# Performance work log

Hardware: AMD Instinct MI355X
Metric: run time of the kernel (lower is better)

## Reference

```python
import jax, jax.numpy as jnp
import numpy as np

NUM_HEADS = 12


def setup_inputs() -> dict:
    key = jax.random.key(0)
    k1, k2, k3, k4 = jax.random.split(key, 4)
    B, N, C = 32, 577, 768
    x = jax.random.normal(k1, (B, N, C), dtype=jnp.float32)
    qkv_w = jax.random.normal(k2, (3 * C, C), dtype=jnp.float32) * 0.02
    proj_w = jax.random.normal(k3, (C, C), dtype=jnp.float32) * 0.02
    proj_b = jax.random.normal(k4, (C,), dtype=jnp.float32) * 0.02
    return {"x": x, "qkv_w": qkv_w, "proj_w": proj_w, "proj_b": proj_b,
            "reduction_num": 115}


def reference(x, qkv_w, proj_w, proj_b, reduction_num):
    B, N, C = x.shape
    H = NUM_HEADS
    hd = C // H
    scale = hd ** -0.5

    # qkv projection (no bias), split into q, k, v of shape (B, H, N, hd)
    qkv = (x @ qkv_w.T).reshape(B, N, 3, H, hd)
    qkv = jnp.transpose(qkv, (2, 0, 3, 1, 4))  # (3, B, H, N, hd)
    q, k, v = qkv[0], qkv[1], qkv[2]

    attn = jax.nn.softmax(jnp.einsum('bhnd,bhmd->bhnm', q * scale, k), axis=-1)  # (B,H,N,N)

    # diagonal entries at positions 1..N-1 (skip CLS), averaged over heads
    attn_diag = jnp.diagonal(attn, axis1=-2, axis2=-1)[:, :, 1:].mean(axis=1)  # (B, N-1)

    token_rank = jnp.argsort(-attn_diag, axis=1)  # descending
    num_kept = N - reduction_num
    kept = token_rank[:, : N - 1 - reduction_num] + 1  # token indices (non-CLS)
    index_cls = jnp.zeros((B, 1), dtype=kept.dtype)
    index_kept = jnp.sort(jnp.concatenate([index_cls, kept], axis=1), axis=1)  # (B, num_kept)

    # gather kept query rows of the attention matrix: (B, H, num_kept, N)
    weight = jnp.take_along_axis(attn, index_kept[:, None, :, None], axis=2)

    out = jnp.einsum('bhkn,bhnd->bhkd', weight, v)  # (B, H, num_kept, hd)
    out = jnp.transpose(out, (0, 2, 1, 3)).reshape(B, num_kept, C)
    out = out @ proj_w.T + proj_b

    original_x = jnp.take_along_axis(x, index_kept[:, :, None], axis=1)  # (B, num_kept, C)
    return out + original_x
```

## Files before the change

### kernel.cpp

```cpp
#include <hip/hip_runtime.h>
#include <math.h>

#define BB_   32
#define NN_   577
#define CC_   768
#define HH_   12
#define HD_   64
#define NPAD  640
#define BH_   (BB_*HH_)
#define MQ    (BB_*NN_)
#define KEPT  462
#define KEPTP 464
#define MP    (BB_*KEPT)
#define TOPK  461

#define MT_   145
#define NT_   18

using short8 = __attribute__((ext_vector_type(8))) short;
using f32x4  = __attribute__((ext_vector_type(4))) float;
using u16x4  = __attribute__((ext_vector_type(4))) unsigned short;
using u32x2  = __attribute__((ext_vector_type(2))) unsigned int;

using gp1_t = const __attribute__((address_space(1))) void*;
using sp3_t = __attribute__((address_space(3))) void*;

__device__ __forceinline__ unsigned short f2bf(float f) {
  unsigned int u = __float_as_uint(f);
  u += 0x7fffu + ((u >> 16) & 1u);
  return (unsigned short)(u >> 16);
}
__device__ __forceinline__ float bf2f(unsigned short h) {
  return __uint_as_float(((unsigned int)h) << 16);
}
__device__ __forceinline__ f32x4 mfma16(short8 a, short8 b, f32x4 c) {
  return __builtin_amdgcn_mfma_f32_16x16x32_bf16(a, b, c, 0, 0, 0);
}
__device__ __forceinline__ void gl_lds16(const void* g, void* l) {
  __builtin_amdgcn_global_load_lds((gp1_t)g, (sp3_t)l, 16, 0, 0);
}

#define SC_ 0.18033688011112042f

__device__ __forceinline__ void split4(const float* __restrict__ in, int i,
                                       unsigned short* __restrict__ hi,
                                       unsigned short* __restrict__ lo) {
  f32x4 f = *(const f32x4*)(in + (size_t)i * 4);
  u16x4 hv, lv;
#pragma unroll
  for (int j = 0; j < 4; ++j) {
    unsigned short h = f2bf(f[j]);
    hv[j] = h;
    lv[j] = f2bf(f[j] - bf2f(h));
  }
  *(u16x4*)(hi + (size_t)i * 4) = hv;
  if (lo) *(u16x4*)(lo + (size_t)i * 4) = lv;
}

#define NX4_ (MQ * 768 / 4)
#define NW4_ (2304 * 768 / 4)
#define NP4_ (768 * 768 / 4)

__global__ __launch_bounds__(256) void k_split_all(
    const float* __restrict__ x, const float* __restrict__ qw,
    const float* __restrict__ pw,
    unsigned short* __restrict__ xh, unsigned short* __restrict__ xl,
    unsigned short* __restrict__ wh, unsigned short* __restrict__ wl,
    unsigned short* __restrict__ pwh) {
  int i = blockIdx.x * 256 + threadIdx.x;
  if (i < NX4_) {
    split4(x, i, xh, xl);
  } else if (i < NX4_ + NW4_) {
    split4(qw, i - NX4_, wh, wl);
  } else if (i < NX4_ + NW4_ + NP4_) {
    split4(pw, i - NX4_ - NW4_, pwh, (unsigned short*)nullptr);
  }
}

__global__ __launch_bounds__(256, 2) void k_qkv(
    const unsigned short* __restrict__ xh, const unsigned short* __restrict__ xl,
    const unsigned short* __restrict__ wh, const unsigned short* __restrict__ wl,
    unsigned short* __restrict__ qh, unsigned short* __restrict__ ql,
    unsigned short* __restrict__ kh, unsigned short* __restrict__ kl,
    unsigned short* __restrict__ vt) {
  __shared__ char smem[65536];
  unsigned short* lAh = (unsigned short*)smem;
  unsigned short* lAl = (unsigned short*)(smem + 16384);
  unsigned short* lBh = (unsigned short*)(smem + 32768);
  unsigned short* lBl = (unsigned short*)(smem + 49152);

  const int tid = threadIdx.x;
  const int wave = tid >> 6, lane = tid & 63, lr = lane & 15, lg = lane >> 4;
  const int wm = wave >> 1, wn = wave & 1;

  const int nwg = MT_ * NT_;
  const int qq = nwg >> 3, rr = nwg & 7;
  int orig = blockIdx.x;
  int xcd = orig & 7, pos = orig >> 3;
  int wgid = (xcd < rr ? xcd * (qq + 1) : rr * (qq + 1) + (xcd - rr) * qq) + pos;
  const int mt = wgid / NT_, nt = wgid - mt * NT_;
  const int m0 = mt * 128, n0 = nt * 128;
  const int which = n0 / 768;
  const bool three = (which < 2);

  f32x4 zf = {0.f, 0.f, 0.f, 0.f};
  f32x4 acc[4][4];
#pragma unroll
  for (int a = 0; a < 4; ++a)
#pragma unroll
    for (int bq = 0; bq < 4; ++bq) acc[a][bq] = zf;

  for (int ks = 0; ks < 12; ++ks) {
    const int k0 = ks * 64;
#pragma unroll
    for (int it = 0; it < 4; ++it) {
      int c = it * 256 + tid;
      int row = c >> 3, slot = c & 7;
      int grow = m0 + row; if (grow > MQ - 1) grow = MQ - 1;
      int gk = k0 + ((slot ^ (row & 7)) << 3);
      gl_lds16(xh + (size_t)grow * 768 + gk,
               (char*)lAh + (it * 256 + wave * 64) * 16);
      if (three)
        gl_lds16(xl + (size_t)grow * 768 + gk,
                 (char*)lAl + (it * 256 + wave * 64) * 16);
    }
#pragma unroll
    for (int it = 0; it < 4; ++it) {
      int c = it * 256 + tid;
      int row = c >> 3, slot = c & 7;
      int gn = n0 + row;
      int gk = k0 + ((slot ^ (row & 7)) << 3);
      gl_lds16(wh + (size_t)gn * 768 + gk,
               (char*)lBh + (it * 256 + wave * 64) * 16);
      if (three)
        gl_lds16(wl + (size_t)gn * 768 + gk,
                 (char*)lBl + (it * 256 + wave * 64) * 16);
    }
    __syncthreads();

#pragma unroll
    for (int kk = 0; kk < 2; ++kk) {
      short8 fa[4], fal[4], fb[4], fbl[4];
#pragma unroll
      for (int ms = 0; ms < 4; ++ms) {
        int row = wm * 64 + ms * 16 + lr;
        int off = (kk * 64 + lg * 16) ^ ((row & 7) << 4);
        fa[ms] = *(const short8*)((const char*)lAh + row * 128 + off);
        if (three) fal[ms] = *(const short8*)((const char*)lAl + row * 128 + off);
      }
#pragma unroll
      for (int ns = 0; ns < 4; ++ns) {
        int row = wn * 64 + ns * 16 + lr;
        int off = (kk * 64 + lg * 16) ^ ((row & 7) << 4);
        fb[ns] = *(const short8*)((const char*)lBh + row * 128 + off);
        if (three) fbl[ns] = *(const short8*)((const char*)lBl + row * 128 + off);
      }
#pragma unroll
      for (int ms = 0; ms < 4; ++ms)
#pragma unroll
        for (int ns = 0; ns < 4; ++ns) {
          acc[ms][ns] = mfma16(fa[ms], fb[ns], acc[ms][ns]);
          if (three) {
            acc[ms][ns] = mfma16(fa[ms], fbl[ns], acc[ms][ns]);
            acc[ms][ns] = mfma16(fal[ms], fb[ns], acc[ms][ns]);
          }
        }
    }
    __syncthreads();
  }

  if (which < 2) {
    float* lC = (float*)smem;
    for (int p = 0; p < 2; ++p) {
      if (p) __syncthreads();
      if (wn == p) {
#pragma unroll
        for (int ms = 0; ms < 4; ++ms)
#pragma unroll
          for (int ns = 0; ns < 4; ++ns) {
            int r = wm * 64 + ms * 16 + 4 * lg;
            int cc = ns * 16 + lr;
#pragma unroll
            for (int reg = 0; reg < 4; ++reg)
              lC[(r + reg) * 66 + cc] = acc[ms][ns][reg];
          }
      }
      __syncthreads();
      const int h = ((n0 % 768) >> 6) + p;
      int r = tid >> 1, c0 = (tid & 1) * 32;
      int m = m0 + r;
      if (m < MQ) {
        int b = m / 577, n = m % 577;
        size_t base = ((size_t)(b * 12 + h) * NPAD + n) * 64 + c0;
        unsigned short* dh = (which == 0 ? qh : kh) + base;
        unsigned short* dl = (which == 0 ? ql : kl) + base;
#pragma unroll
        for (int cc = 0; cc < 32; cc += 4) {
          u16x4 hv, lv;
#pragma unroll
          for (int j = 0; j < 4; ++j) {
            float f = lC[r * 66 + c0 + cc + j];
            unsigned short hh = f2bf(f);
            hv[j] = hh;
            lv[j] = f2bf(f - bf2f(hh));
          }
          *(u16x4*)(dh + cc) = hv;
          *(u16x4*)(dl + cc) = lv;
        }
      }
    }
  } else {
    const int h0 = (n0 % 768) >> 6;
#pragma unroll
    for (int ms = 0; ms < 4; ++ms)
#pragma unroll
      for (int ns = 0; ns < 4; ++ns) {
        int m = m0 + wm * 64 + ms * 16 + 4 * lg;
        int c = wn * 64 + ns * 16 + lr;
        int h = h0 + (c >> 6), d = c & 63;
        int b = m / 577, n = m - b * 577;
        if (m + 3 < MQ && n + 3 < 577) {
          u16x4 pv;
#pragma unroll
          for (int reg = 0; reg < 4; ++reg) pv[reg] = f2bf(acc[ms][ns][reg]);
          *(u16x4*)(vt + ((size_t)(b * 12 + h) * 64 + d) * NPAD + n) = pv;
        } else {
#pragma unroll
          for (int reg = 0; reg < 4; ++reg) {
            int mm = m + reg;
            if (mm < MQ) {
              int bb = mm / 577, nn = mm - bb * 577;
              vt[((size_t)(bb * 12 + h) * 64 + d) * NPAD + nn] = f2bf(acc[ms][ns][reg]);
            }
          }
        }
      }
  }
}

__global__ __launch_bounds__(256) void k_attn1(
    const unsigned short* __restrict__ qh, const unsigned short* __restrict__ ql,
    const unsigned short* __restrict__ kh, const unsigned short* __restrict__ kl,
    const unsigned short* __restrict__ vt, float* __restrict__ S0,
    float* __restrict__ Dg, unsigned short* __restrict__ Ob) {
  __shared__ char smem[34816];
  char* lK = smem;
  char* lV = smem + 16384;
  char* lP = smem + 24576;

  int wgid = (blockIdx.x & 7) * 480 + (blockIdx.x >> 3);
  const int bh = wgid / 10;
  const int i0 = (wgid - bh * 10) * 64;
  const int tid = threadIdx.x, w = tid >> 6, lane = tid & 63;
  const int lr = lane & 15, lg = lane >> 4;
  const size_t qb = (size_t)bh * NPAD * 64;

  const int krow = tid >> 3, kslot = tid & 7;
  const int vrow = tid >> 2, vslot = tid & 3;
  const size_t ksrc = (size_t)krow * 64 + ((kslot ^ (krow & 7)) << 3);
  const size_t vsrc = ((size_t)bh * 64 + vrow) * NPAD + ((vslot ^ (vrow & 3)) << 3);

  short8 qf[2], qfl[2];
  {
    const size_t qrow = qb + (size_t)(i0 + w * 16 + lr) * 64;
#pragma unroll
    for (int kk = 0; kk < 2; ++kk) {
      qf[kk]  = *(const short8*)(qh + qrow + kk * 32 + lg * 8);
      qfl[kk] = *(const short8*)(ql + qrow + kk * 32 + lg * 8);
    }
  }
  f32x4 zf = {0.f, 0.f, 0.f, 0.f};
  f32x4 oacc[4];
#pragma unroll
  for (int ds = 0; ds < 4; ++ds) oacc[ds] = zf;
  float s0 = 0.0f;

  gl_lds16(kh + qb + ksrc, lK + tid * 16);
  gl_lds16(kl + qb + ksrc, lK + 4096 + tid * 16);
  gl_lds16(vt + vsrc, lV + tid * 16);
  __syncthreads();

  int buf = 0, pb = 0;
  char* lPw = lP + w * 2560;
  for (int jp = 0; jp < 19; ++jp) {
    if (jp < 18) {
      int jn = (jp + 1) * 32;
      gl_lds16(kh + qb + (size_t)jn * 64 + ksrc, lK + (buf ^ 1) * 8192 + tid * 16);
      gl_lds16(kl + qb + (size_t)jn * 64 + ksrc, lK + (buf ^ 1) * 8192 + 4096 + tid * 16);
      gl_lds16(vt + vsrc + jn, lV + (buf ^ 1) * 4096 + tid * 16);
    }
#pragma unroll
    for (int t = 0; t < 2; ++t) {
      const int jloc = t * 16 + lr;
      short8 kfh[2], kfl2[2];
#pragma unroll
      for (int kk = 0; kk < 2; ++kk) {
        int off = (kk * 64 + lg * 16) ^ ((jloc & 7) << 4);
        kfh[kk]  = *(const short8*)(lK + buf * 8192 + jloc * 128 + off);
        kfl2[kk] = *(const short8*)(lK + buf * 8192 + 4096 + jloc * 128 + off);
      }
      f32x4 c = zf;
#pragma unroll
      for (int kk = 0; kk < 2; ++kk) {
        c = mfma16(kfh[kk], qfl[kk], c);
        c = mfma16(kfl2[kk], qf[kk], c);
        c = mfma16(kfh[kk], qf[kk], c);
      }
      int jbase = jp * 32 + t * 16 + 4 * lg;
      float p0 = (jbase + 0 < 577) ? exp2f(c[0] * SC_) : 0.0f;
      float p1 = (jbase + 1 < 577) ? exp2f(c[1] * SC_) : 0.0f;
      float p2 = (jbase + 2 < 577) ? exp2f(c[2] * SC_) : 0.0f;
      float p3 = (jbase + 3 < 577) ? exp2f(c[3] * SC_) : 0.0f;
      s0 += (p0 + p1) + (p2 + p3);
      u32x2 wv;
      wv[0] = (unsigned)f2bf(p0) | ((unsigned)f2bf(p1) << 16);
      wv[1] = (unsigned)f2bf(p2) | ((unsigned)f2bf(p3) << 16);
      *(u32x2*)(lPw + pb * 1280 + lr * 80 + t * 32 + lg * 8) = wv;
    }
    asm volatile("" ::: "memory");
    short8 pa = *(const short8*)(lPw + pb * 1280 + lr * 80 + lg * 16);
#pragma unroll
    for (int ds = 0; ds < 4; ++ds) {
      int r = ds * 16 + lr;
      int off = (lg * 16) ^ ((r & 3) << 4);
      short8 vf = *(const short8*)(lV + buf * 4096 + r * 64 + off);
      oacc[ds] = mfma16(pa, vf, oacc[ds]);
    }
    asm volatile("" ::: "memory");
    pb ^= 1;
    __syncthreads();
    buf ^= 1;
  }

  s0 += __shfl_xor(s0, 16);
  s0 += __shfl_xor(s0, 32);
  const int iw = i0 + w * 16;
  if (lg == 0) S0[(size_t)bh * NPAD + iw + lr] = s0;
  float rs[4];
#pragma unroll
  for (int reg = 0; reg < 4; ++reg) rs[reg] = 1.0f / __shfl(s0, 4 * lg + reg);
#pragma unroll
  for (int ds = 0; ds < 4; ++ds)
#pragma unroll
    for (int reg = 0; reg < 4; ++reg)
      Ob[((size_t)bh * NPAD + iw + 4 * lg + reg) * 64 + ds * 16 + lr] =
          f2bf(oacc[ds][reg] * rs[reg]);

  {
    const int row = i0 + (tid >> 2);
    const int c = tid & 3;
    const size_t base = qb + (size_t)row * 64 + c * 16;
    short8 a0 = *(const short8*)(qh + base), a1 = *(const short8*)(qh + base + 8);
    short8 b0 = *(const short8*)(ql + base), b1 = *(const short8*)(ql + base + 8);
    short8 c0 = *(const short8*)(kh + base), c1 = *(const short8*)(kh + base + 8);
    short8 d0 = *(const short8*)(kl + base), d1 = *(const short8*)(kl + base + 8);
    float acc = 0.0f;
#pragma unroll
    for (int j = 0; j < 8; ++j) {
      float qv = bf2f((unsigned short)a0[j]) + bf2f((unsigned short)b0[j]);
      float kv = bf2f((unsigned short)c0[j]) + bf2f((unsigned short)d0[j]);
      acc += qv * kv;
      float qv1 = bf2f((unsigned short)a1[j]) + bf2f((unsigned short)b1[j]);
      float kv1 = bf2f((unsigned short)c1[j]) + bf2f((unsigned short)d1[j]);
      acc += qv1 * kv1;
    }
    acc += __shfl_xor(acc, 1, 4);
    acc += __shfl_xor(acc, 2, 4);
    if (c == 0) Dg[(size_t)bh * NPAD + row] = acc * SC_;
  }
}

__global__ __launch_bounds__(576) void k_select(const float* __restrict__ Dg,
                                                const float* __restrict__ S0,
                                                int* __restrict__ idxk) {
  __shared__ float kbuf[576];
  __shared__ int kflag[576];
  int b = blockIdx.x, t = threadIdx.x;
  if (t < 576) {
    float a = 0.0f;
#pragma unroll
    for (int h = 0; h < 12; ++h) {
      size_t o = (size_t)(b * 12 + h) * NPAD + t + 1;
      a += exp2f(Dg[o]) / S0[o];
    }
    kbuf[t] = a;
  }
  __syncthreads();
  if (t < 576) {
    float kt = kbuf[t];
    int cnt = 0;
    for (int j = 0; j < 576; ++j) {
      float kj = kbuf[j];
      cnt += (kj > kt || (kj == kt && j < t)) ? 1 : 0;
    }
    kflag[t] = (cnt < TOPK) ? 1 : 0;
  }
  __syncthreads();
  if (t < 576 && kflag[t]) {
    int pos = 1;
    for (int j = 0; j < t; ++j) pos += kflag[j];
    idxk[b * KEPTP + pos] = t + 1;
  }
  if (t == 0) {
    idxk[b * KEPTP + 0] = 0;
    idxk[b * KEPTP + 462] = 0;
    idxk[b * KEPTP + 463] = 0;
  }
}

__global__ __launch_bounds__(256) void k_proj(
    const unsigned short* __restrict__ Ob, const unsigned short* __restrict__ pwh,
    const float* __restrict__ pb, const float* __restrict__ x,
    const int* __restrict__ idxk, float* __restrict__ out) {
  __shared__ char smem[33792];
  unsigned short* lA = (unsigned short*)smem;
  unsigned short* lB = (unsigned short*)(smem + 16384);
  const int tid = threadIdx.x;
  const int wave = tid >> 6, lane = tid & 63, lr = lane & 15, lg = lane >> 4;
  const int wm = wave >> 1, wn = wave & 1;
  int wgid = (blockIdx.x & 7) * 87 + (blockIdx.x >> 3);
  const int mt = wgid / 6, nt = wgid - mt * 6;
  const int m0 = mt * 128, n0 = nt * 128;

  int tokr[4], bbr[4], offr8[4];
#pragma unroll
  for (int it = 0; it < 4; ++it) {
    int c = it * 256 + tid;
    int row = c >> 3, slot = c & 7;
    int m = m0 + row; if (m > MP - 1) m = MP - 1;
    int bb = m / 462, tt = m - bb * 462;
    tokr[it] = idxk[bb * KEPTP + tt];
    bbr[it] = bb;
    offr8[it] = (slot ^ (row & 7)) << 3;
  }

  f32x4 zf = {0.f, 0.f, 0.f, 0.f};
  f32x4 acc[4][4];
#pragma unroll
  for (int a = 0; a < 4; ++a)
#pragma unroll
    for (int bq = 0; bq < 4; ++bq) acc[a][bq] = zf;

  for (int ks = 0; ks < 12; ++ks) {
    int k0 = ks * 64;
#pragma unroll
    for (int it = 0; it < 4; ++it) {
      gl_lds16(Ob + ((size_t)(bbr[it] * 12 + ks) * NPAD + tokr[it]) * 64 + offr8[it],
               (char*)lA + (it * 256 + wave * 64) * 16);
    }
#pragma unroll
    for (int it = 0; it < 4; ++it) {
      int c = it * 256 + tid;
      int row = c >> 3, slot = c & 7;
      int gk = k0 + ((slot ^ (row & 7)) << 3);
      gl_lds16(pwh + (size_t)(n0 + row) * 768 + gk,
               (char*)lB + (it * 256 + wave * 64) * 16);
    }
    __syncthreads();
#pragma unroll
    for (int kk = 0; kk < 2; ++kk) {
      short8 fa[4], fb[4];
#pragma unroll
      for (int ms = 0; ms < 4; ++ms) {
        int row = wm * 64 + ms * 16 + lr;
        int off = (kk * 64 + lg * 16) ^ ((row & 7) << 4);
        fa[ms] = *(const short8*)((const char*)lA + row * 128 + off);
      }
#pragma unroll
      for (int ns = 0; ns < 4; ++ns) {
        int row = wn * 64 + ns * 16 + lr;
        int off = (kk * 64 + lg * 16) ^ ((row & 7) << 4);
        fb[ns] = *(const short8*)((const char*)lB + row * 128 + off);
      }
#pragma unroll
      for (int ms = 0; ms < 4; ++ms)
#pragma unroll
        for (int ns = 0; ns < 4; ++ns)
          acc[ms][ns] = mfma16(fa[ms], fb[ns], acc[ms][ns]);
    }
    __syncthreads();
  }

  float* lC = (float*)smem;
  for (int p = 0; p < 2; ++p) {
    if (p) __syncthreads();
    if (wn == p) {
#pragma unroll
      for (int ms = 0; ms < 4; ++ms)
#pragma unroll
        for (int ns = 0; ns < 4; ++ns) {
          int r = wm * 64 + ms * 16 + 4 * lg;
          int cc = ns * 16 + lr;
#pragma unroll
          for (int reg = 0; reg < 4; ++reg)
            lC[(r + reg) * 66 + cc] = acc[ms][ns][reg];
        }
    }
    __syncthreads();
    int r = tid >> 1, c0 = (tid & 1) * 32;
    int m = m0 + r;
    if (m < MP) {
      int bb = m / 462, tt = m % 462;
      int tok = idxk[bb * KEPTP + tt];
      int col = n0 + p * 64 + c0;
      const float* xs = x + ((size_t)(bb * 577) + tok) * 768 + col;
      float* dst = out + (size_t)m * 768 + col;
#pragma unroll
      for (int cc = 0; cc < 32; cc += 4) {
        f32x4 xv = *(const f32x4*)(xs + cc);
        f32x4 bv = *(const f32x4*)(pb + col + cc);
        f32x4 o;
#pragma unroll
        for (int j = 0; j < 4; ++j)
          o[j] = lC[r * 66 + c0 + cc + j] + bv[j] + xv[j];
        *(f32x4*)(dst + cc) = o;
      }
    }
  }
}

extern "C" void kernel_launch(void* const* d_in, const int* in_sizes, int n_in,
                              void* d_out, int out_size, void* d_ws, size_t ws_size,
                              hipStream_t stream) {
  const float* x  = (const float*)d_in[0];
  const float* qw = (const float*)d_in[1];
  const float* pw = (const float*)d_in[2];
  const float* pb = (const float*)d_in[3];
  (void)in_sizes; (void)n_in; (void)out_size; (void)ws_size;

  char* ws = (char*)d_ws;
  size_t off = 0;
  auto alloc = [&](size_t bytes) {
    void* p = ws + off;
    off += (bytes + 255) & ~(size_t)255;
    return p;
  };
  unsigned short* xh  = (unsigned short*)alloc((size_t)MQ * 768 * 2);
  unsigned short* xl  = (unsigned short*)alloc((size_t)MQ * 768 * 2);
  unsigned short* wh  = (unsigned short*)alloc((size_t)2304 * 768 * 2);
  unsigned short* wl  = (unsigned short*)alloc((size_t)2304 * 768 * 2);
  unsigned short* pwh = (unsigned short*)alloc((size_t)768 * 768 * 2);
  unsigned short* qhp = (unsigned short*)alloc((size_t)BH_ * NPAD * 64 * 2);
  unsigned short* qlp = (unsigned short*)alloc((size_t)BH_ * NPAD * 64 * 2);
  unsigned short* khp = (unsigned short*)alloc((size_t)BH_ * NPAD * 64 * 2);
  unsigned short* klp = (unsigned short*)alloc((size_t)BH_ * NPAD * 64 * 2);
  unsigned short* vtp = (unsigned short*)alloc((size_t)BH_ * NPAD * 64 * 2);
  unsigned short* Obf = (unsigned short*)alloc((size_t)BH_ * NPAD * 64 * 2);
  float* S0  = (float*)alloc((size_t)BH_ * NPAD * 4);
  float* Dg  = (float*)alloc((size_t)BH_ * NPAD * 4);
  int*   idxk = (int*)alloc((size_t)BB_ * KEPTP * 4);

  k_split_all<<<dim3((NX4_ + NW4_ + NP4_ + 255) / 256), 256, 0, stream>>>(
      x, qw, pw, xh, xl, wh, wl, pwh);
  k_qkv<<<dim3(MT_ * NT_), 256, 0, stream>>>(xh, xl, wh, wl, qhp, qlp, khp, klp, vtp);
  k_attn1<<<dim3(3840), 256, 0, stream>>>(qhp, qlp, khp, klp, vtp, S0, Dg, Obf);
  k_select<<<dim3(32), 576, 0, stream>>>(Dg, S0, idxk);
  k_proj<<<dim3(696), 256, 0, stream>>>(Obf, pwh, pb, x, idxk, (float*)d_out);
}
```

Baseline: 377.6 us.

## Double query rows per attention workgroup to reuse K/V tiles; two elements per split thread

After: 377.1 us, median of 3. About the same (-0.1%).

```diff
diff --git a/kernel.cpp b/kernel.cpp
--- a/kernel.cpp
+++ b/kernel.cpp
@@ -67,13 +67,17 @@
     unsigned short* __restrict__ xh, unsigned short* __restrict__ xl,
     unsigned short* __restrict__ wh, unsigned short* __restrict__ wl,
     unsigned short* __restrict__ pwh) {
-  int i = blockIdx.x * 256 + threadIdx.x;
-  if (i < NX4_) {
-    split4(x, i, xh, xl);
-  } else if (i < NX4_ + NW4_) {
-    split4(qw, i - NX4_, wh, wl);
-  } else if (i < NX4_ + NW4_ + NP4_) {
-    split4(pw, i - NX4_ - NW4_, pwh, (unsigned short*)nullptr);
+  int i2 = blockIdx.x * 256 + threadIdx.x;
+#pragma unroll
+  for (int s = 0; s < 2; ++s) {
+    int i = 2 * i2 + s;
+    if (i < NX4_) {
+      split4(x, i, xh, xl);
+    } else if (i < NX4_ + NW4_) {
+      split4(qw, i - NX4_, wh, wl);
+    } else if (i < NX4_ + NW4_ + NP4_) {
+      split4(pw, i - NX4_ - NW4_, pwh, (unsigned short*)nullptr);
+    }
   }
 }
 
@@ -243,14 +247,14 @@
     const unsigned short* __restrict__ kh, const unsigned short* __restrict__ kl,
     const unsigned short* __restrict__ vt, float* __restrict__ S0,
     float* __restrict__ Dg, unsigned short* __restrict__ Ob) {
-  __shared__ char smem[34816];
+  __shared__ char smem[45056];
   char* lK = smem;
   char* lV = smem + 16384;
   char* lP = smem + 24576;
 
-  int wgid = (blockIdx.x & 7) * 480 + (blockIdx.x >> 3);
-  const int bh = wgid / 10;
-  const int i0 = (wgid - bh * 10) * 64;
+  int wgid = (blockIdx.x & 7) * 240 + (blockIdx.x >> 3);
+  const int bh = wgid / 5;
+  const int i0 = (wgid - bh * 5) * 128;
   const int tid = threadIdx.x, w = tid >> 6, lane = tid & 63;
   const int lr = lane & 15, lg = lane >> 4;
   const size_t qb = (size_t)bh * NPAD * 64;
@@ -260,20 +264,23 @@
   const size_t ksrc = (size_t)krow * 64 + ((kslot ^ (krow & 7)) << 3);
   const size_t vsrc = ((size_t)bh * 64 + vrow) * NPAD + ((vslot ^ (vrow & 3)) << 3);
 
-  short8 qf[2], qfl[2];
-  {
-    const size_t qrow = qb + (size_t)(i0 + w * 16 + lr) * 64;
+  short8 qf[2][2], qfl[2][2];
+#pragma unroll
+  for (int iu = 0; iu < 2; ++iu) {
+    const size_t qrow = qb + (size_t)(i0 + w * 32 + iu * 16 + lr) * 64;
 #pragma unroll
     for (int kk = 0; kk < 2; ++kk) {
-      qf[kk]  = *(const short8*)(qh + qrow + kk * 32 + lg * 8);
-      qfl[kk] = *(const short8*)(ql + qrow + kk * 32 + lg * 8);
+      qf[iu][kk]  = *(const short8*)(qh + qrow + kk * 32 + lg * 8);
+      qfl[iu][kk] = *(const short8*)(ql + qrow + kk * 32 + lg * 8);
     }
   }
   f32x4 zf = {0.f, 0.f, 0.f, 0.f};
-  f32x4 oacc[4];
-#pragma unroll
-  for (int ds = 0; ds < 4; ++ds) oacc[ds] = zf;
-  float s0 = 0.0f;
+  f32x4 oacc[2][4];
+#pragma unroll
+  for (int iu = 0; iu < 2; ++iu)
+#pragma unroll
+    for (int ds = 0; ds < 4; ++ds) oacc[iu][ds] = zf;
+  float s0[2] = {0.0f, 0.0f};
 
   gl_lds16(kh + qb + ksrc, lK + tid * 16);
   gl_lds16(kl + qb + ksrc, lK + 4096 + tid * 16);
@@ -281,7 +288,7 @@
   __syncthreads();
 
   int buf = 0, pb = 0;
-  char* lPw = lP + w * 2560;
+  char* lPw = lP + w * 5120;
   for (int jp = 0; jp < 19; ++jp) {
     if (jp < 18) {
       int jn = (jp + 1) * 32;
@@ -299,32 +306,38 @@
         kfh[kk]  = *(const short8*)(lK + buf * 8192 + jloc * 128 + off);
         kfl2[kk] = *(const short8*)(lK + buf * 8192 + 4096 + jloc * 128 + off);
       }
-      f32x4 c = zf;
-#pragma unroll
-      for (int kk = 0; kk < 2; ++kk) {
-        c = mfma16(kfh[kk], qfl[kk], c);
-        c = mfma16(kfl2[kk], qf[kk], c);
-        c = mfma16(kfh[kk], qf[kk], c);
-      }
       int jbase = jp * 32 + t * 16 + 4 * lg;
-      float p0 = (jbase + 0 < 577) ? exp2f(c[0] * SC_) : 0.0f;
-      float p1 = (jbase + 1 < 577) ? exp2f(c[1] * SC_) : 0.0f;
-      float p2 = (jbase + 2 < 577) ? exp2f(c[2] * SC_) : 0.0f;
-      float p3 = (jbase + 3 < 577) ? exp2f(c[3] * SC_) : 0.0f;
-      s0 += (p0 + p1) + (p2 + p3);
-      u32x2 wv;
-      wv[0] = (unsigned)f2bf(p0) | ((unsigned)f2bf(p1) << 16);
-      wv[1] = (unsigned)f2bf(p2) | ((unsigned)f2bf(p3) << 16);
-      *(u32x2*)(lPw + pb * 1280 + lr * 80 + t * 32 + lg * 8) = wv;
+#pragma unroll
+      for (int iu = 0; iu < 2; ++iu) {
+        f32x4 c = zf;
+#pragma unroll
+        for (int kk = 0; kk < 2; ++kk) {
+          c = mfma16(kfh[kk], qfl[iu][kk], c);
+          c = mfma16(kfl2[kk], qf[iu][kk], c);
+          c = mfma16(kfh[kk], qf[iu][kk], c);
+        }
+        float p0 = (jbase + 0 < 577) ? exp2f(c[0] * SC_) : 0.0f;
+        float p1 = (jbase + 1 < 577) ? exp2f(c[1] * SC_) : 0.0f;
+        float p2 = (jbase + 2 < 577) ? exp2f(c[2] * SC_) : 0.0f;
+        float p3 = (jbase + 3 < 577) ? exp2f(c[3] * SC_) : 0.0f;
+        s0[iu] += (p0 + p1) + (p2 + p3);
+        u32x2 wv;
+        wv[0] = (unsigned)f2bf(p0) | ((unsigned)f2bf(p1) << 16);
+        wv[1] = (unsigned)f2bf(p2) | ((unsigned)f2bf(p3) << 16);
+        *(u32x2*)(lPw + iu * 2560 + pb * 1280 + lr * 80 + t * 32 + lg * 8) = wv;
+      }
     }
     asm volatile("" ::: "memory");
-    short8 pa = *(const short8*)(lPw + pb * 1280 + lr * 80 + lg * 16);
-#pragma unroll
-    for (int ds = 0; ds < 4; ++ds) {
-      int r = ds * 16 + lr;
-      int off = (lg * 16) ^ ((r & 3) << 4);
-      short8 vf = *(const short8*)(lV + buf * 4096 + r * 64 + off);
-      oacc[ds] = mfma16(pa, vf, oacc[ds]);
+#pragma unroll
+    for (int iu = 0; iu < 2; ++iu) {
+      short8 pa = *(const short8*)(lPw + iu * 2560 + pb * 1280 + lr * 80 + lg * 16);
+#pragma unroll
+      for (int ds = 0; ds < 4; ++ds) {
+        int r = ds * 16 + lr;
+        int off = (lg * 16) ^ ((r & 3) << 4);
+        short8 vf = *(const short8*)(lV + buf * 4096 + r * 64 + off);
+        oacc[iu][ds] = mfma16(pa, vf, oacc[iu][ds]);
+      }
     }
     asm volatile("" ::: "memory");
     pb ^= 1;
@@ -332,22 +345,27 @@
     buf ^= 1;
   }
 
-  s0 += __shfl_xor(s0, 16);
-  s0 += __shfl_xor(s0, 32);
-  const int iw = i0 + w * 16;
-  if (lg == 0) S0[(size_t)bh * NPAD + iw + lr] = s0;
-  float rs[4];
-#pragma unroll
-  for (int reg = 0; reg < 4; ++reg) rs[reg] = 1.0f / __shfl(s0, 4 * lg + reg);
-#pragma unroll
-  for (int ds = 0; ds < 4; ++ds)
-#pragma unroll
-    for (int reg = 0; reg < 4; ++reg)
-      Ob[((size_t)bh * NPAD + iw + 4 * lg + reg) * 64 + ds * 16 + lr] =
-          f2bf(oacc[ds][reg] * rs[reg]);
-
-  {
-    const int row = i0 + (tid >> 2);
+#pragma unroll
+  for (int iu = 0; iu < 2; ++iu) {
+    float s = s0[iu];
+    s += __shfl_xor(s, 16);
+    s += __shfl_xor(s, 32);
+    const int iw = i0 + w * 32 + iu * 16;
+    if (lg == 0) S0[(size_t)bh * NPAD + iw + lr] = s;
+    float rs[4];
+#pragma unroll
+    for (int reg = 0; reg < 4; ++reg) rs[reg] = 1.0f / __shfl(s, 4 * lg + reg);
+#pragma unroll
+    for (int ds = 0; ds < 4; ++ds)
+#pragma unroll
+      for (int reg = 0; reg < 4; ++reg)
+        Ob[((size_t)bh * NPAD + iw + 4 * lg + reg) * 64 + ds * 16 + lr] =
+            f2bf(oacc[iu][ds][reg] * rs[reg]);
+  }
+
+#pragma unroll
+  for (int rr = 0; rr < 2; ++rr) {
+    const int row = i0 + rr * 64 + (tid >> 2);
     const int c = tid & 3;
     const size_t base = qb + (size_t)row * 64 + c * 16;
     short8 a0 = *(const short8*)(qh + base), a1 = *(const short8*)(qh + base + 8);
@@ -550,10 +568,10 @@
   float* Dg  = (float*)alloc((size_t)BH_ * NPAD * 4);
   int*   idxk = (int*)alloc((size_t)BB_ * KEPTP * 4);
 
-  k_split_all<<<dim3((NX4_ + NW4_ + NP4_ + 255) / 256), 256, 0, stream>>>(
+  k_split_all<<<dim3(((NX4_ + NW4_ + NP4_) / 2 + 255) / 256), 256, 0, stream>>>(
       x, qw, pw, xh, xl, wh, wl, pwh);
   k_qkv<<<dim3(MT_ * NT_), 256, 0, stream>>>(xh, xl, wh, wl, qhp, qlp, khp, klp, vtp);
-  k_attn1<<<dim3(3840), 256, 0, stream>>>(qhp, qlp, khp, klp, vtp, S0, Dg, Obf);
+  k_attn1<<<dim3(1920), 256, 0, stream>>>(qhp, qlp, khp, klp, vtp, S0, Dg, Obf);
   k_select<<<dim3(32), 576, 0, stream>>>(Dg, S0, idxk);
   k_proj<<<dim3(696), 256, 0, stream>>>(Obf, pwh, pb, x, idxk, (float*)d_out);
 }
```
